# Kernel tuning notes

Measured on AMD Instinct MI355X. Metric: run time of the kernel, lower is better.

## Reference

```python
import jax, jax.numpy as jnp
import numpy as np

N_NODES = 100000
N_EDGES = 1600000
IN_CH, HID_CH, OUT_CH = 64, 64, 16
N_REL = 8


def setup_inputs() -> dict:
    key = jax.random.key(0)
    ks = jax.random.split(key, 10)
    x = jax.random.normal(ks[0], (N_NODES, IN_CH), dtype=jnp.float32)
    edge_index = jax.random.randint(ks[1], (2, N_EDGES), 0, N_NODES, dtype=jnp.int64)
    edge_type = jax.random.randint(ks[2], (N_EDGES,), 0, N_REL, dtype=jnp.int64)
    # RGCNConv params: per-relation weight, root weight, bias (Glorot-ish scale)
    def glorot(k, shape):
        fan = shape[-2] + shape[-1]
        return jax.random.normal(k, shape, dtype=jnp.float32) * jnp.sqrt(2.0 / fan)
    W1 = glorot(ks[3], (N_REL, IN_CH, HID_CH))
    root1 = glorot(ks[4], (IN_CH, HID_CH))
    b1 = jnp.zeros((HID_CH,), dtype=jnp.float32)
    W2 = glorot(ks[5], (N_REL, HID_CH, OUT_CH))
    root2 = glorot(ks[6], (HID_CH, OUT_CH))
    b2 = jnp.zeros((OUT_CH,), dtype=jnp.float32)
    return {"x": x, "edge_index": edge_index, "edge_type": edge_type,
            "W1": W1, "root1": root1, "b1": b1,
            "W2": W2, "root2": root2, "b2": b2}


def rgcn_conv(x, src, dst, edge_type, W_rel, W_root, bias):
    """PyG RGCNConv: out_i = x_i @ W_root + b + sum_r mean_{j in N_r(i)} x_j @ W_r.
    Mean is linear, so aggregate raw features per relation, then transform."""
    n = x.shape[0]
    xs = x[src]  # [E, F] gathered source features (hot memory-bound op)
    out = x @ W_root + bias
    for r in range(W_rel.shape[0]):  # small fixed relation count
        mask = (edge_type == r).astype(x.dtype)  # [E]
        agg = jax.ops.segment_sum(xs * mask[:, None], dst, num_segments=n)  # [N, F]
        cnt = jax.ops.segment_sum(mask, dst, num_segments=n)  # [N]
        agg = agg / jnp.clip(cnt, 1.0)[:, None]  # mean aggr; 0 when no edges
        out = out + agg @ W_rel[r]
    return out


def reference(x, edge_index, edge_type, W1, root1, b1, W2, root2, b2):
    src, dst = edge_index[0], edge_index[1]
    h = rgcn_conv(x, src, dst, edge_type, W1, root1, b1)
    h = jax.nn.relu(h)
    h = rgcn_conv(h, src, dst, edge_type, W2, root2, b2)
    # global_mean_pool with a single graph: mean over nodes -> [1, out]
    g = jnp.mean(h, axis=0, keepdims=True)
    return jax.nn.log_softmax(g, axis=1)
```

## Files before the change

### kernel.cpp

```cpp
#include <hip/hip_runtime.h>
#include <hip/hip_bf16.h>


#define CH 64
#define BK_EDGES 2048
#define CAP 12288
#define RPT 12
#define KB 128
#define KRB 1024

typedef __attribute__((ext_vector_type(8))) short short8;
typedef __attribute__((ext_vector_type(4))) float f32x4;
typedef __attribute__((ext_vector_type(2))) float f32x2;

__device__ inline ushort f2bf(float f) {
    unsigned b = __float_as_uint(f);
    unsigned r = (b + 0x7FFFu + ((b >> 16) & 1u)) >> 16;
    return (ushort)r;
}
__device__ inline float bf2f(ushort u) {
    return __uint_as_float(((unsigned)u) << 16);
}

__device__ inline void acc8fp8(float* a, uint2 w, float m) {
    f32x2 p;
    p = __builtin_amdgcn_cvt_pk_f32_fp8(w.x, 0); a[0] += m * p.x; a[1] += m * p.y;
    p = __builtin_amdgcn_cvt_pk_f32_fp8(w.x, 1); a[2] += m * p.x; a[3] += m * p.y;
    p = __builtin_amdgcn_cvt_pk_f32_fp8(w.y, 0); a[4] += m * p.x; a[5] += m * p.y;
    p = __builtin_amdgcn_cvt_pk_f32_fp8(w.y, 1); a[6] += m * p.x; a[7] += m * p.y;
}


__global__ __launch_bounds__(256) void prep_kernel(
    const int* __restrict__ src, const int* __restrict__ dst,
    const int* __restrict__ etype,
    int* __restrict__ gBucketCnt, int2* __restrict__ bucket_buf,
    int E, int N)
{
    __shared__ int s_k[BK_EDGES];
    __shared__ int s_y[BK_EDGES];
    __shared__ int hist[256], scanv[256], lcur[256], bstart[256], gbase[256];
    const int t = threadIdx.x;
    const int bid = blockIdx.x;

    const int e0 = bid * BK_EDGES;
    const int cnt = min(BK_EDGES, E - e0);

    hist[t] = 0;
    __syncthreads();

    int myb[8], myk[8], myy[8];
    #pragma unroll
    for (int i = 0; i < 8; ++i) {
        int li = t + i * 256;
        if (li < cnt) {
            int e = e0 + li;
            int r = etype[e];
            int k = r * N + dst[e];
            myk[i] = k;
            myy[i] = (r << 17) | src[e];
            myb[i] = k >> 12;
            atomicAdd(&hist[myb[i]], 1);
        } else myb[i] = -1;
    }
    __syncthreads();

    int v = hist[t];
    scanv[t] = v;
    __syncthreads();
    for (int off = 1; off < 256; off <<= 1) {
        int u = (t >= off) ? scanv[t - off] : 0;
        __syncthreads();
        scanv[t] += u;
        __syncthreads();
    }
    int excl = scanv[t] - v;
    bstart[t] = excl;
    lcur[t] = excl;
    __syncthreads();

    #pragma unroll
    for (int i = 0; i < 8; ++i) {
        if (myb[i] >= 0) {
            int p = atomicAdd(&lcur[myb[i]], 1);
            s_k[p] = myk[i];
            s_y[p] = myy[i];
        }
    }
    __syncthreads();

    if (v > 0) gbase[t] = atomicAdd(&gBucketCnt[t], v);
    __syncthreads();

    for (int p = t; p < cnt; p += 256) {
        int k = s_k[p];
        int b = k >> 12;
        int gp = gbase[b] + (p - bstart[b]);
        if (gp < CAP)
            bucket_buf[(size_t)b * CAP + gp] = make_int2(k, s_y[p]);
    }
}


__global__ __launch_bounds__(1024) void build_kernel(
    const int2* __restrict__ bucket_buf, const int* __restrict__ gBucketCnt,
    int* __restrict__ rowptr, float* __restrict__ inv,
    int* __restrict__ perm,
    const float* __restrict__ x, const float* __restrict__ W1,
    const float* __restrict__ root1,
    ushort* __restrict__ xbf, unsigned char* __restrict__ xq,
    ushort* __restrict__ wf,
    int N, int nbuk, int nXbf)
{
    __shared__ int hist[4096];
    __shared__ int cur[4096];
    __shared__ int part[1024];
    const int t = threadIdx.x;
    const int bid = blockIdx.x;

    if (bid >= nbuk) {
        int cb = bid - nbuk;
        if (cb < nXbf) {
            int i = cb * 1024 + t;
            if (i < N * CH / 4) {
                float4 v = ((const float4*)x)[i];
                ((ushort4*)xbf)[i] = make_ushort4(f2bf(v.x), f2bf(v.y), f2bf(v.z), f2bf(v.w));
                int p8 = __builtin_amdgcn_cvt_pk_fp8_f32(v.x, v.y, 0, 0);
                p8 = __builtin_amdgcn_cvt_pk_fp8_f32(v.z, v.w, p8, 1);
                ((unsigned int*)xq)[i] = (unsigned int)p8;
            }
        } else {
            int idx = (cb - nXbf) * 1024 + t;
            if (idx < 9 * 2 * 4 * 64 * 8) {
                int j    = idx & 7;
                int lane = (idx >> 3) & 63;
                int ct   = (idx >> 9) & 3;
                int ks   = (idx >> 11) & 1;
                int rel  = idx >> 12;
                int k = ks * 32 + (lane >> 4) * 8 + j;
                int n = ct * 16 + (lane & 15);
                float v = (rel < 8) ? W1[((size_t)rel * 64 + k) * 64 + n]
                                    : root1[(size_t)k * 64 + n];
                wf[idx] = f2bf(v);
            }
        }
        return;
    }

    const int b = bid;
    const int nb = min(gBucketCnt[b], CAP);
    const int2* rec = bucket_buf + (size_t)b * CAP;

    int rk[RPT], ry[RPT];
    #pragma unroll
    for (int i = 0; i < RPT; ++i) {
        int j = t + i * 1024;
        if (j < nb) { int2 v = rec[j]; rk[i] = v.x; ry[i] = v.y; }
        else        { rk[i] = -1; ry[i] = 0; }
    }

    int bc = (t < 256) ? gBucketCnt[t] : 0;
    part[t] = bc;
    __syncthreads();
    for (int off = 1; off < 1024; off <<= 1) {
        int u = (t >= off) ? part[t - off] : 0;
        __syncthreads();
        part[t] += u;
        __syncthreads();
    }
    __shared__ int baseS;
    if (t == b) baseS = part[t] - bc;
    __syncthreads();
    const int base = baseS;

    for (int i = t; i < 4096; i += 1024) hist[i] = 0;
    __syncthreads();
    #pragma unroll
    for (int i = 0; i < RPT; ++i)
        if (rk[i] >= 0) atomicAdd(&hist[rk[i] & 4095], 1);
    __syncthreads();

    const int i0 = t * 4;
    int h0 = hist[i0], h1 = hist[i0 + 1], h2 = hist[i0 + 2], h3 = hist[i0 + 3];
    int s = h0 + h1 + h2 + h3;
    part[t] = s;
    __syncthreads();
    for (int off = 1; off < 1024; off <<= 1) {
        int u = (t >= off) ? part[t - off] : 0;
        __syncthreads();
        part[t] += u;
        __syncthreads();
    }
    int run = base + part[t] - s;
    int hk[4] = {h0, h1, h2, h3};
    #pragma unroll
    for (int k = 0; k < 4; ++k) {
        cur[i0 + k] = run;
        rowptr[b * 4096 + i0 + k] = run;
        inv[b * 4096 + i0 + k] = 1.0f / (float)max(hk[k], 1);
        run += hk[k];
    }
    __syncthreads();

    #pragma unroll
    for (int i = 0; i < RPT; ++i) {
        if (rk[i] >= 0) {
            int pos = atomicAdd(&cur[rk[i] & 4095], 1);
            perm[pos] = ry[i] & 0x1FFFF;
        }
    }
}


__global__ __launch_bounds__(256) void rgcn1_fused_kernel(
    const int* __restrict__ rowptr, const int* __restrict__ perm,
    const float* __restrict__ inv, const ushort* __restrict__ xbf,
    const unsigned char* __restrict__ xq,
    const ushort* __restrict__ wfrag, const float* __restrict__ b1,
    const int2* __restrict__ bucket_buf, const int* __restrict__ gBucketCnt,
    float* __restrict__ kappa,
    ushort* __restrict__ h, int N, int nbuk)
{
    if (blockIdx.x < KB) {
        for (int b = blockIdx.x; b < nbuk; b += KB) {
            const int nb = min(gBucketCnt[b], CAP);
            const int2* rec = bucket_buf + (size_t)b * CAP;
            for (int j = (int)threadIdx.x; j < nb; j += 256) {
                int2 v = rec[j];
                float iv = inv[v.x];
                unsafeAtomicAdd(&kappa[((v.y & 0x1FFFF) << 3) | (v.y >> 17)], iv);
            }
        }
        return;
    }

    __shared__ ushort Abuf[4][16 * 72];
    __shared__ int    rpS[4][144];
    __shared__ float  invS[4][128];
    const int widx = threadIdx.x >> 6;
    const int lane = threadIdx.x & 63;
    const int wid = ((blockIdx.x - KB) << 2) | widx;
    const int base = wid << 4;
    if (base >= N) return;

    const int m0 = lane & 15;
    const int q  = lane >> 4;
    const int sg = lane >> 3;
    const int cg = lane & 7;
    ushort* ab = Abuf[widx];
    int*    rpL = rpS[widx];
    float*  ivL = invS[widx];

    for (int i = lane; i < 136; i += 64) {
        int r = i / 17, mm = i - r * 17;
        rpL[i] = rowptr[(size_t)r * N + base + mm];
    }
    for (int i = lane; i < 128; i += 64)
        ivL[i] = inv[(size_t)(i >> 4) * N + base + (i & 15)];

    f32x4 acc4[4];
    #pragma unroll
    for (int ct = 0; ct < 4; ++ct) acc4[ct] = (f32x4)(0.0f);

    for (int r = 0; r < 8; ++r) {
        const int iA = r * 17 + sg;
        const int iB = iA + 8;
        int jA = rpL[iA], eA = rpL[iA + 1];
        int jB = rpL[iB], eB = rpL[iB + 1];
        float a[8] = {}, bacc[8] = {};
        int s0A = perm[(jA     < eA) ? jA     : 0];
        int s1A = perm[(jA + 1 < eA) ? jA + 1 : 0];
        int s0B = perm[(jB     < eB) ? jB     : 0];
        int s1B = perm[(jB + 1 < eB) ? jB + 1 : 0];
        while (jA < eA || jB < eB) {
            uint2 w0A = *(const uint2*)(xq + (size_t)s0A * CH + (cg << 3));
            uint2 w1A = *(const uint2*)(xq + (size_t)s1A * CH + (cg << 3));
            uint2 w0B = *(const uint2*)(xq + (size_t)s0B * CH + (cg << 3));
            uint2 w1B = *(const uint2*)(xq + (size_t)s1B * CH + (cg << 3));
            int t0A = perm[(jA + 2 < eA) ? jA + 2 : 0];
            int t1A = perm[(jA + 3 < eA) ? jA + 3 : 0];
            int t0B = perm[(jB + 2 < eB) ? jB + 2 : 0];
            int t1B = perm[(jB + 3 < eB) ? jB + 3 : 0];
            float m0A = (jA     < eA) ? 1.f : 0.f;
            float m1A = (jA + 1 < eA) ? 1.f : 0.f;
            float m0B = (jB     < eB) ? 1.f : 0.f;
            float m1B = (jB + 1 < eB) ? 1.f : 0.f;
            acc8fp8(a,    w0A, m0A);
            acc8fp8(a,    w1A, m1A);
            acc8fp8(bacc, w0B, m0B);
            acc8fp8(bacc, w1B, m1B);
            s0A = t0A; s1A = t1A; s0B = t0B; s1B = t1B;
            jA += 2; jB += 2;
        }
        const float ivA = ivL[(r << 4) | sg];
        const float ivB = ivL[(r << 4) | (8 + sg)];
        short8 oA, oB;
        #pragma unroll
        for (int k = 0; k < 8; ++k) {
            oA[k] = (short)f2bf(a[k] * ivA);
            oB[k] = (short)f2bf(bacc[k] * ivB);
        }
        *(short8*)&ab[sg * 72 + (cg << 3)]       = oA;
        *(short8*)&ab[(8 + sg) * 72 + (cg << 3)] = oB;

        #pragma unroll
        for (int s = 0; s < 2; ++s) {
            short8 av = *(short8*)&ab[m0 * 72 + s * 32 + q * 8];
            #pragma unroll
            for (int ct = 0; ct < 4; ++ct) {
                short8 bv = *(const short8*)&wfrag[(((size_t)(r * 2 + s) * 4 + ct) * 64 + lane) * 8];
                acc4[ct] = __builtin_amdgcn_mfma_f32_16x16x32_bf16(av, bv, acc4[ct], 0, 0, 0);
            }
        }
    }

    {
        int node = min(base + m0, N - 1);
        #pragma unroll
        for (int s = 0; s < 2; ++s) {
            short8 av = *(const short8*)&xbf[(size_t)node * CH + s * 32 + q * 8];
            #pragma unroll
            for (int ct = 0; ct < 4; ++ct) {
                short8 bv = *(const short8*)&wfrag[(((size_t)(8 * 2 + s) * 4 + ct) * 64 + lane) * 8];
                acc4[ct] = __builtin_amdgcn_mfma_f32_16x16x32_bf16(av, bv, acc4[ct], 0, 0, 0);
            }
        }
    }

    #pragma unroll
    for (int ct = 0; ct < 4; ++ct) {
        int c = ct * 16 + m0;
        float bb = b1[c];
        #pragma unroll
        for (int v = 0; v < 4; ++v) {
            int node = base + q * 4 + v;
            if (node < N)
                h[(size_t)node * CH + c] = f2bf(fmaxf(acc4[ct][v] + bb, 0.f));
        }
    }
}


__global__ __launch_bounds__(256) void kred_kernel(
    const ushort* __restrict__ h, const float* __restrict__ kappa,
    float* __restrict__ partial, int N)
{
    const int lane = threadIdx.x & 63;
    const int w = threadIdx.x >> 6;
    int wave = (blockIdx.x << 2) | w;
    const int wstride = gridDim.x << 2;
    float racc[9] = {};
    for (int i = wave; i < N; i += wstride) {
        float hv = bf2f(h[(size_t)i * CH + lane]);
        #pragma unroll
        for (int r = 0; r < 8; ++r) racc[r] += hv * kappa[i * 8 + r];
        racc[8] += hv;
    }
    __shared__ float red[4][9][64];
    #pragma unroll
    for (int r = 0; r < 9; ++r) red[w][r][lane] = racc[r];
    __syncthreads();
    if (w == 0) {
        #pragma unroll
        for (int r = 0; r < 9; ++r) {
            float s4 = red[0][r][lane] + red[1][r][lane] + red[2][r][lane] + red[3][r][lane];
            partial[(size_t)blockIdx.x * 576 + r * 64 + lane] = s4;
        }
    }
}


__global__ __launch_bounds__(576) void kred2_kernel(
    const float* __restrict__ partial, float* __restrict__ sacc, int nblk)
{
    const int j = threadIdx.x;
    const int chunk = nblk >> 3;
    const int b0 = blockIdx.x * chunk;
    float s = 0.f;
    for (int b = b0; b < b0 + chunk; b += 4) {
        float v0 = partial[(size_t)b * 576 + j];
        float v1 = partial[(size_t)(b + 1) * 576 + j];
        float v2 = partial[(size_t)(b + 2) * 576 + j];
        float v3 = partial[(size_t)(b + 3) * 576 + j];
        s += (v0 + v1) + (v2 + v3);
    }
    unsafeAtomicAdd(&sacc[j], s);
}

__global__ void finalize_kernel(const float* __restrict__ sacc, const float* __restrict__ root2,
                                const float* __restrict__ W2, const float* __restrict__ b2,
                                float* __restrict__ out, float invN)
{
    __shared__ float g[16];
    int t = threadIdx.x;
    if (t < 16) {
        const float* s0 = sacc + 512;
        float acc = 0.f;
        for (int c = 0; c < 64; ++c) acc += s0[c] * root2[c * 16 + t];
        for (int r = 0; r < 8; ++r) {
            const float* sr = sacc + r * 64;
            for (int c = 0; c < 64; ++c) acc += sr[c] * W2[(r * 64 + c) * 16 + t];
        }
        g[t] = acc * invN + b2[t];
    }
    __syncthreads();
    if (t < 16) {
        float m = -1e30f;
        for (int i = 0; i < 16; ++i) m = fmaxf(m, g[i]);
        float s = 0.f;
        for (int i = 0; i < 16; ++i) s += expf(g[i] - m);
        out[t] = g[t] - (m + logf(s));
    }
}


extern "C" void kernel_launch(void* const* d_in, const int* in_sizes, int n_in,
                              void* d_out, int out_size, void* d_ws, size_t ws_size,
                              hipStream_t stream)
{
    const float* x     = (const float*)d_in[0];
    const int*   eidx  = (const int*)d_in[1];
    const int*   etype = (const int*)d_in[2];
    const float* W1    = (const float*)d_in[3];
    const float* root1 = (const float*)d_in[4];
    const float* b1    = (const float*)d_in[5];
    const float* W2    = (const float*)d_in[6];
    const float* root2 = (const float*)d_in[7];
    const float* b2    = (const float*)d_in[8];
    float* out = (float*)d_out;

    const int E = in_sizes[1] / 2;
    const int N = in_sizes[0] / CH;
    const int NKEY = N * 8;
    const int NBUK = (NKEY + 4095) / 4096;
    const int KSPACE = NBUK << 12;
    const int* srcI = eidx;
    const int* dstI = eidx + E;

    int* wsi = (int*)d_ws;
    int*   gBucketCnt = wsi;
    float* sacc       = (float*)(gBucketCnt + 256);
    float* kappa      = sacc + 576;
    float* inv        = kappa + NKEY;
    int*   rowptr     = (int*)(inv + KSPACE);
    int*   perm       = rowptr + KSPACE + 16;
    size_t off = (size_t)((perm + E) - wsi);
    off = (off + 1) & ~(size_t)1;
    int2*  bucket_buf = (int2*)(wsi + off);
    off += (size_t)NBUK * CAP * 2;
    off = (off + 7) & ~(size_t)7;
    ushort* xbf = (ushort*)(wsi + off);
    ushort* wfg = xbf + (size_t)N * CH;
    unsigned char* xq = (unsigned char*)(wfg + 36864);
    ushort* h = (ushort*)(xq + (size_t)N * CH);
    float* partial = (float*)(h + (size_t)N * CH);

    hipMemsetAsync(d_ws, 0, (size_t)(256 + 576 + NKEY) * 4, stream);

    const int nBin = (E + BK_EDGES - 1) / BK_EDGES;
    prep_kernel<<<nBin, 256, 0, stream>>>(
        srcI, dstI, etype, gBucketCnt, bucket_buf, E, N);

    const int nXbf = (N * CH / 4 + 1023) / 1024;
    const int nWf  = (36864 + 1023) / 1024;
    build_kernel<<<NBUK + nXbf + nWf, 1024, 0, stream>>>(
        bucket_buf, gBucketCnt, rowptr, inv, perm,
        x, W1, root1, xbf, xq, wfg, N, NBUK, nXbf);

    const int tiles = (N + 15) / 16;
    rgcn1_fused_kernel<<<KB + (tiles + 3) / 4, 256, 0, stream>>>(
        rowptr, perm, inv, xbf, xq, wfg, b1, bucket_buf, gBucketCnt, kappa,
        h, N, NBUK);

    kred_kernel<<<KRB, 256, 0, stream>>>(h, kappa, partial, N);
    kred2_kernel<<<8, 576, 0, stream>>>(partial, sacc, KRB);
    finalize_kernel<<<1, 64, 0, stream>>>(sacc, root2, W2, b2, out, 1.0f / (float)N);
}
```

Before: 278.2 us.

## Drop bf16 x copy, zero kappa in build, fuse finalize into kred2

Removes the separate bf16 copy of x and instead decodes the fp8 copy into bf16 for the root-weight MFMA, cutting one full-size write and later read of node features. Moves the kappa zeroing from the host memset into the build kernel, which shrinks the memset to a few counters. Fuses the finalize kernel into kred2 using a last-block-done atomic counter, removing one launch. The root term now uses fp8-precision features, so accuracy drops slightly.

```diff
diff --git a/kernel.cpp b/kernel.cpp
--- a/kernel.cpp
+++ b/kernel.cpp
@@ -28,6 +28,19 @@
     p = __builtin_amdgcn_cvt_pk_f32_fp8(w.x, 1); a[2] += m * p.x; a[3] += m * p.y;
     p = __builtin_amdgcn_cvt_pk_f32_fp8(w.y, 0); a[4] += m * p.x; a[5] += m * p.y;
     p = __builtin_amdgcn_cvt_pk_f32_fp8(w.y, 1); a[6] += m * p.x; a[7] += m * p.y;
+}
+
+__device__ inline short8 dec8fp8(uint2 w) {
+    float f[8];
+    f32x2 p;
+    p = __builtin_amdgcn_cvt_pk_f32_fp8(w.x, 0); f[0] = p.x; f[1] = p.y;
+    p = __builtin_amdgcn_cvt_pk_f32_fp8(w.x, 1); f[2] = p.x; f[3] = p.y;
+    p = __builtin_amdgcn_cvt_pk_f32_fp8(w.y, 0); f[4] = p.x; f[5] = p.y;
+    p = __builtin_amdgcn_cvt_pk_f32_fp8(w.y, 1); f[6] = p.x; f[7] = p.y;
+    short8 r;
+    #pragma unroll
+    for (int k = 0; k < 8; ++k) r[k] = (short)f2bf(f[k]);
+    return r;
 }
 
 
@@ -108,8 +121,8 @@
     int* __restrict__ perm,
     const float* __restrict__ x, const float* __restrict__ W1,
     const float* __restrict__ root1,
-    ushort* __restrict__ xbf, unsigned char* __restrict__ xq,
-    ushort* __restrict__ wf,
+    unsigned char* __restrict__ xq, ushort* __restrict__ wf,
+    float* __restrict__ kappa, int nkey,
     int N, int nbuk, int nXbf)
 {
     __shared__ int hist[4096];
@@ -124,7 +137,6 @@
             int i = cb * 1024 + t;
             if (i < N * CH / 4) {
                 float4 v = ((const float4*)x)[i];
-                ((ushort4*)xbf)[i] = make_ushort4(f2bf(v.x), f2bf(v.y), f2bf(v.z), f2bf(v.w));
                 int p8 = __builtin_amdgcn_cvt_pk_fp8_f32(v.x, v.y, 0, 0);
                 p8 = __builtin_amdgcn_cvt_pk_fp8_f32(v.z, v.w, p8, 1);
                 ((unsigned int*)xq)[i] = (unsigned int)p8;
@@ -151,6 +163,9 @@
     const int nb = min(gBucketCnt[b], CAP);
     const int2* rec = bucket_buf + (size_t)b * CAP;
 
+    for (int i = b * 1024 + t; i < nkey; i += nbuk * 1024)
+        kappa[i] = 0.0f;
+
     int rk[RPT], ry[RPT];
     #pragma unroll
     for (int i = 0; i < RPT; ++i) {
@@ -214,7 +229,7 @@
 
 __global__ __launch_bounds__(256) void rgcn1_fused_kernel(
     const int* __restrict__ rowptr, const int* __restrict__ perm,
-    const float* __restrict__ inv, const ushort* __restrict__ xbf,
+    const float* __restrict__ inv,
     const unsigned char* __restrict__ xq,
     const ushort* __restrict__ wfrag, const float* __restrict__ b1,
     const int2* __restrict__ bucket_buf, const int* __restrict__ gBucketCnt,
@@ -318,7 +333,8 @@
         int node = min(base + m0, N - 1);
         #pragma unroll
         for (int s = 0; s < 2; ++s) {
-            short8 av = *(const short8*)&xbf[(size_t)node * CH + s * 32 + q * 8];
+            uint2 wv = *(const uint2*)(xq + (size_t)node * CH + s * 32 + q * 8);
+            short8 av = dec8fp8(wv);
             #pragma unroll
             for (int ct = 0; ct < 4; ++ct) {
                 short8 bv = *(const short8*)&wfrag[(((size_t)(8 * 2 + s) * 4 + ct) * 64 + lane) * 8];
@@ -371,7 +387,11 @@
 
 
 __global__ __launch_bounds__(576) void kred2_kernel(
-    const float* __restrict__ partial, float* __restrict__ sacc, int nblk)
+    const float* __restrict__ partial, float* __restrict__ sacc,
+    int* __restrict__ done,
+    const float* __restrict__ root2, const float* __restrict__ W2,
+    const float* __restrict__ b2, float* __restrict__ out,
+    float invN, int nblk)
 {
     const int j = threadIdx.x;
     const int chunk = nblk >> 3;
@@ -385,31 +405,32 @@
         s += (v0 + v1) + (v2 + v3);
     }
     unsafeAtomicAdd(&sacc[j], s);
-}
-
-__global__ void finalize_kernel(const float* __restrict__ sacc, const float* __restrict__ root2,
-                                const float* __restrict__ W2, const float* __restrict__ b2,
-                                float* __restrict__ out, float invN)
-{
+    __threadfence();
+    __syncthreads();
+    __shared__ int tk;
+    if (j == 0) tk = atomicAdd(done, 1);
+    __syncthreads();
+    if (tk != 7) return;
+    __threadfence();
+
     __shared__ float g[16];
-    int t = threadIdx.x;
-    if (t < 16) {
+    if (j < 16) {
         const float* s0 = sacc + 512;
         float acc = 0.f;
-        for (int c = 0; c < 64; ++c) acc += s0[c] * root2[c * 16 + t];
+        for (int c = 0; c < 64; ++c) acc += s0[c] * root2[c * 16 + j];
         for (int r = 0; r < 8; ++r) {
             const float* sr = sacc + r * 64;
-            for (int c = 0; c < 64; ++c) acc += sr[c] * W2[(r * 64 + c) * 16 + t];
-        }
-        g[t] = acc * invN + b2[t];
-    }
-    __syncthreads();
-    if (t < 16) {
+            for (int c = 0; c < 64; ++c) acc += sr[c] * W2[(r * 64 + c) * 16 + j];
+        }
+        g[j] = acc * invN + b2[j];
+    }
+    __syncthreads();
+    if (j < 16) {
         float m = -1e30f;
         for (int i = 0; i < 16; ++i) m = fmaxf(m, g[i]);
-        float s = 0.f;
-        for (int i = 0; i < 16; ++i) s += expf(g[i] - m);
-        out[t] = g[t] - (m + logf(s));
+        float sm = 0.f;
+        for (int i = 0; i < 16; ++i) sm += expf(g[i] - m);
+        out[j] = g[j] - (m + logf(sm));
     }
 }
 
@@ -440,7 +461,8 @@
     int* wsi = (int*)d_ws;
     int*   gBucketCnt = wsi;
     float* sacc       = (float*)(gBucketCnt + 256);
-    float* kappa      = sacc + 576;
+    int*   done       = (int*)(sacc + 576);
+    float* kappa      = (float*)(done + 16);
     float* inv        = kappa + NKEY;
     int*   rowptr     = (int*)(inv + KSPACE);
     int*   perm       = rowptr + KSPACE + 16;
@@ -449,13 +471,12 @@
     int2*  bucket_buf = (int2*)(wsi + off);
     off += (size_t)NBUK * CAP * 2;
     off = (off + 7) & ~(size_t)7;
-    ushort* xbf = (ushort*)(wsi + off);
-    ushort* wfg = xbf + (size_t)N * CH;
+    ushort* wfg = (ushort*)(wsi + off);
     unsigned char* xq = (unsigned char*)(wfg + 36864);
     ushort* h = (ushort*)(xq + (size_t)N * CH);
     float* partial = (float*)(h + (size_t)N * CH);
 
-    hipMemsetAsync(d_ws, 0, (size_t)(256 + 576 + NKEY) * 4, stream);
+    hipMemsetAsync(d_ws, 0, (size_t)(256 + 576 + 16) * 4, stream);
 
     const int nBin = (E + BK_EDGES - 1) / BK_EDGES;
     prep_kernel<<<nBin, 256, 0, stream>>>(
@@ -465,14 +486,15 @@
     const int nWf  = (36864 + 1023) / 1024;
     build_kernel<<<NBUK + nXbf + nWf, 1024, 0, stream>>>(
         bucket_buf, gBucketCnt, rowptr, inv, perm,
-        x, W1, root1, xbf, xq, wfg, N, NBUK, nXbf);
+        x, W1, root1, xq, wfg, kappa, NKEY, N, NBUK, nXbf);
 
     const int tiles = (N + 15) / 16;
     rgcn1_fused_kernel<<<KB + (tiles + 3) / 4, 256, 0, stream>>>(
-        rowptr, perm, inv, xbf, xq, wfg, b1, bucket_buf, gBucketCnt, kappa,
+        rowptr, perm, inv, xq, wfg, b1, bucket_buf, gBucketCnt, kappa,
         h, N, NBUK);
 
     kred_kernel<<<KRB, 256, 0, stream>>>(h, kappa, partial, N);
-    kred2_kernel<<<8, 576, 0, stream>>>(partial, sacc, KRB);
-    finalize_kernel<<<1, 64, 0, stream>>>(sacc, root2, W2, b2, out, 1.0f / (float)N);
-}
+    kred2_kernel<<<8, 576, 0, stream>>>(partial, sacc, done,
+                                        root2, W2, b2, out,
+                                        1.0f / (float)N, KRB);
+}
```

After: 270.6 us (median of 3 runs). -2.7%, faster.
